# Kernel optimization log

Measured on AMD Instinct MI355X. Metric: run time of the kernel, lower is better.

## Reference

```python
import jax, jax.numpy as jnp
import numpy as np

BETA, GAMMA, ZETA = 0.66, -0.1, 1.1  # hard-concrete params
N, E, S = 20000, 640000, 256          # nodes, edges, samples (node feature dim)
D, P, PH, OUT = 2000, 500, 100, 2     # DEmRNA, pathway, pathway-hidden, out nodes


def setup_inputs() -> dict:
    key = jax.random.key(0)
    ks = jax.random.split(key, 14)
    return {
        "lnc_data": jax.random.normal(ks[0], (S, 8000), jnp.float32),
        "mi_data": jax.random.normal(ks[1], (S, 2000), jnp.float32),
        "m_data": jax.random.normal(ks[2], (S, 10000), jnp.float32),
        "src": jax.random.randint(ks[3], (E,), 0, N, dtype=jnp.int32),
        "dst": jax.random.randint(ks[4], (E,), 0, N, dtype=jnp.int32),
        "demrna_index": jax.random.randint(ks[5], (D,), 0, N, dtype=jnp.int32),
        "attn_l": jax.random.normal(ks[6], (N, 1), jnp.float32) * 0.01,
        "attn_r": jax.random.normal(ks[7], (N, 1), jnp.float32) * 0.01,
        "bias_l0": jnp.zeros((1,), jnp.float32),
        "pathway_mask": (jax.random.uniform(ks[8], (P, D)) < 0.1).astype(jnp.float32),
        "W_mp": jax.random.normal(ks[9], (P, D), jnp.float32) * (1.414 / np.sqrt(D)),
        "b_mp": jnp.zeros((P,), jnp.float32),
        "W_ph": jax.random.normal(ks[10], (PH, P), jnp.float32) * 0.05,
        "b_ph": jnp.zeros((PH,), jnp.float32),
        "W_po": jax.random.normal(ks[11], (OUT, PH), jnp.float32) * 0.1,
        "b_po": jnp.zeros((OUT,), jnp.float32),
    }


def _standardize(x):
    # torch pre_process: per-column (dim 0) mean/std, std unbiased (ddof=1)
    return (x - x.mean(axis=0)) / x.std(axis=0, ddof=1)


def reference(lnc_data, mi_data, m_data, src, dst, demrna_index,
              attn_l, attn_r, bias_l0, pathway_mask,
              W_mp, b_mp, W_ph, b_ph, W_po, b_po):
    rna = jnp.concatenate([lnc_data, mi_data, m_data], axis=1)  # [S, N]
    a_rna = _standardize(rna.T)                                  # [N, S] node feats

    # per-node attention logits (attn_l/r broadcast over sample dim)
    a1 = (a_rna * attn_l).sum(-1, keepdims=True)                 # [N, 1]
    a2 = (a_rna * attn_r).sum(-1, keepdims=True)                 # [N, 1]

    # edge attention with hard-concrete L0 gate (eval / l0_test path)
    logits = a1[src] + a2[dst] + bias_l0                         # [E, 1]
    s = jax.nn.sigmoid(logits / BETA)
    a = jnp.clip(s * (ZETA - GAMMA) + GAMMA, 0.0, 1.0)

    # custom edge-softmax: normalize by per-dst sum of gates
    z = jax.ops.segment_sum(a, dst, num_segments=N)              # [N, 1]
    a = a / z[dst]
    a = jnp.where(jnp.isnan(a), 0.0, a)                          # 0/0 -> 0

    # two rounds of u_mul_e + sum scatter aggregation
    rna1 = jax.ops.segment_sum(a * a_rna[src], dst, num_segments=N)  # [N, S]
    rna2 = jax.ops.segment_sum(a * rna1[src], dst, num_segments=N)   # [N, S]

    x = (a_rna + rna1 + rna2).T[:, demrna_index]                 # [S, D]

    # pas_net pathway branch (weight masked by pathway_mask each forward)
    h = jax.nn.relu(x @ (W_mp * pathway_mask).T + b_mp)          # [S, P]
    h = jax.nn.relu(h @ W_ph.T + b_ph)                           # [S, PH]
    return jax.nn.softmax(h @ W_po.T + b_po, axis=1)             # [S, OUT]
```

## Files before the change

### kernel.cpp

```cpp
#include <hip/hip_runtime.h>

#define NN 20000
#define EE 640000
#define SS 256
#define DD 2000
#define PP 500
#define PHH 100
#define ZSPLIT 25
#define KCH 80
#define SUB 10

typedef unsigned short ushort_t;

__device__ __forceinline__ unsigned short f2bf(float f) {
  unsigned u = __float_as_uint(f);
  unsigned r = (u + 0x7FFFu + ((u >> 16) & 1u)) >> 16;
  return (unsigned short)r;
}
__device__ __forceinline__ float lo16(unsigned u) { return __uint_as_float(u << 16); }
__device__ __forceinline__ float hi16(unsigned u) { return __uint_as_float(u & 0xFFFF0000u); }

__global__ __launch_bounds__(256) void k_meanstd(
    const float* __restrict__ lnc, const float* __restrict__ mi,
    const float* __restrict__ mdat, float* __restrict__ mean,
    float* __restrict__ invstd) {
  int s = blockIdx.x, tid = threadIdx.x;
  double sum = 0.0, ssq = 0.0;
  const float4* L = (const float4*)(lnc + (size_t)s * 8000);
  const float4* M = (const float4*)(mi + (size_t)s * 2000);
  const float4* D = (const float4*)(mdat + (size_t)s * 10000);
  for (int i = tid; i < 2000; i += 256) {
    float4 v = L[i];
    sum += (double)v.x + (double)v.y + (double)v.z + (double)v.w;
    ssq += (double)v.x * v.x + (double)v.y * v.y + (double)v.z * v.z + (double)v.w * v.w;
  }
  for (int i = tid; i < 500; i += 256) {
    float4 v = M[i];
    sum += (double)v.x + (double)v.y + (double)v.z + (double)v.w;
    ssq += (double)v.x * v.x + (double)v.y * v.y + (double)v.z * v.z + (double)v.w * v.w;
  }
  for (int i = tid; i < 2500; i += 256) {
    float4 v = D[i];
    sum += (double)v.x + (double)v.y + (double)v.z + (double)v.w;
    ssq += (double)v.x * v.x + (double)v.y * v.y + (double)v.z * v.z + (double)v.w * v.w;
  }
  __shared__ double sm[256], sq[256];
  sm[tid] = sum; sq[tid] = ssq; __syncthreads();
  for (int o = 128; o > 0; o >>= 1) {
    if (tid < o) { sm[tid] += sm[tid + o]; sq[tid] += sq[tid + o]; }
    __syncthreads();
  }
  if (tid == 0) {
    double mu = sm[0] / 20000.0;
    double var = (sq[0] - 20000.0 * mu * mu) / 19999.0;
    mean[s] = (float)mu;
    invstd[s] = (float)(1.0 / sqrt(var));
  }
}

__global__ __launch_bounds__(256) void k_prep(
    const float* __restrict__ lnc, const float* __restrict__ mi,
    const float* __restrict__ mdat, const float* __restrict__ mean,
    const float* __restrict__ invstd, ushort_t* __restrict__ a_rna,
    float* __restrict__ rowsum4, const float* __restrict__ Wmp,
    const float* __restrict__ pmask, float* __restrict__ Wt,
    int* __restrict__ counts) {
  int b = blockIdx.x;
  int tx = threadIdx.x, ty = threadIdx.y;
  if (b < 2500) {
    __shared__ float tile[64][33];
    __shared__ float red[8][33];
    int nb = (b % 625) * 32, sb = (b / 625) * 64;
    int n = nb + tx;
    const float* base; int w, c;
    if (n < 8000)       { base = lnc;  w = 8000;  c = n; }
    else if (n < 10000) { base = mi;   w = 2000;  c = n - 8000; }
    else                { base = mdat; w = 10000; c = n - 10000; }
    for (int r = ty; r < 64; r += 8) {
      int s = sb + r;
      tile[r][tx] = (base[(size_t)s * w + c] - mean[s]) * invstd[s];
    }
    __syncthreads();
    float ps = 0.f;
    for (int r = ty; r < 64; r += 8) ps += tile[r][tx];
    red[ty][tx] = ps;
    __syncthreads();
    if (ty == 0) {
      float t = 0.f;
      #pragma unroll
      for (int j = 0; j < 8; ++j) t += red[j][tx];
      rowsum4[(size_t)(sb >> 6) * NN + nb + tx] = t;
    }
    ushort2* out2 = (ushort2*)a_rna;
    for (int r2 = ty; r2 < 32; r2 += 8) {
      int nn = nb + r2;
      ushort2 v;
      v.x = f2bf(tile[2 * tx][r2]);
      v.y = f2bf(tile[2 * tx + 1][r2]);
      out2[(size_t)nn * 128 + (sb >> 1) + tx] = v;
    }
  } else if (b < 3508) {
    __shared__ float tile[32][33];
    int b2 = b - 2500;
    int p0 = (b2 & 15) * 32, d0 = (b2 >> 4) * 32;
    for (int r = ty; r < 32; r += 8) {
      int p = p0 + r, d = d0 + tx;
      float v = 0.f;
      if (p < PP && d < DD) v = Wmp[(size_t)p * DD + d] * pmask[(size_t)p * DD + d];
      tile[r][tx] = v;
    }
    __syncthreads();
    for (int r = ty; r < 32; r += 8) {
      int d = d0 + r, p = p0 + tx;
      if (d < DD) Wt[(size_t)d * 512 + p] = tile[tx][r];
    }
  } else {
    int b3 = b - 3508;
    int idx = b3 * 256 + ty * 32 + tx;
    if (idx < NN / 4) {
      uint4 z; z.x = 0; z.y = 0; z.z = 0; z.w = 0;
      ((uint4*)counts)[idx] = z;
    }
  }
}

__global__ __launch_bounds__(256) void k_count2(
    const int* __restrict__ dst, int* __restrict__ counts,
    const float* __restrict__ rowsum4, const float* __restrict__ attnl,
    const float* __restrict__ attnr, float* __restrict__ a1, float* __restrict__ a2) {
  int b = blockIdx.x;
  if (b < 2500) {
    int e = b * 256 + threadIdx.x;
    if (e < EE) atomicAdd(&counts[dst[e]], 1);
  } else {
    int n = (b - 2500) * 256 + threadIdx.x;
    if (n < NN) {
      float t = rowsum4[n] + rowsum4[NN + n] + rowsum4[2 * NN + n] + rowsum4[3 * NN + n];
      a1[n] = attnl[n] * t;
      a2[n] = attnr[n] * t;
    }
  }
}

__global__ __launch_bounds__(1024) void k_scan(
    const int* __restrict__ counts, int* __restrict__ offsets, int* __restrict__ cursor) {
  __shared__ int sums[1024];
  int t = threadIdx.x;
  int base = t * 20;
  int local[20];
  int s = 0;
  for (int i = 0; i < 20; ++i) {
    int idx = base + i;
    int c = (idx < NN) ? counts[idx] : 0;
    local[i] = s; s += c;
  }
  sums[t] = s; __syncthreads();
  for (int d = 1; d < 1024; d <<= 1) {
    int v = (t >= d) ? sums[t - d] : 0;
    __syncthreads();
    sums[t] += v;
    __syncthreads();
  }
  int prefix = (t > 0) ? sums[t - 1] : 0;
  for (int i = 0; i < 20; ++i) {
    int idx = base + i;
    if (idx < NN) { int o = prefix + local[i]; offsets[idx] = o; cursor[idx] = o; }
  }
  if (t == 1023) offsets[NN] = sums[1023];
}

__device__ __forceinline__ float hc_gate(float l) {
  float sg = 1.0f / (1.0f + __expf(-l * 1.5151515151f));
  return fminf(fmaxf(fmaf(sg, 1.2f, -0.1f), 0.0f), 1.0f);
}

__global__ __launch_bounds__(256) void k_fill(
    const int* __restrict__ src, const int* __restrict__ dst,
    const float* __restrict__ a1, const float* __restrict__ a2,
    const float* __restrict__ bias0, int* __restrict__ cursor,
    uint2* __restrict__ csr) {
  int e = blockIdx.x * 256 + threadIdx.x;
  if (e >= EE) return;
  int d = dst[e], s = src[e];
  float a = hc_gate(a1[s] + a2[d] + bias0[0]);
  int slot = atomicAdd(&cursor[d], 1);
  uint2 rec; rec.x = (unsigned)s; rec.y = __float_as_uint(a);
  csr[slot] = rec;
}

__global__ __launch_bounds__(256) void k_agg(
    const uint2* __restrict__ csr, const int* __restrict__ offs,
    const ushort_t* __restrict__ in_bf, ushort_t* __restrict__ out_bf,
    float* __restrict__ zinv) {
  int wave = threadIdx.x >> 6, lane = threadIdx.x & 63;
  int half = lane >> 5, sl = lane & 31;
  int n = blockIdx.x * 4 + wave;
  int beg = __builtin_amdgcn_readfirstlane(offs[n]);
  int end = __builtin_amdgcn_readfirstlane(offs[n + 1]);
  float zp = 0.f;
  for (int i = beg + lane; i < end; i += 64) zp += __uint_as_float(csr[i].y);
  #pragma unroll
  for (int o = 1; o < 64; o <<= 1) zp += __shfl_xor(zp, o, 64);
  float inv = (zp > 0.f) ? 1.0f / zp : 0.0f;
  if (lane == 0) zinv[n] = inv;

  const uint4* in4 = (const uint4*)in_bf;
  float acc[8] = {0.f, 0.f, 0.f, 0.f, 0.f, 0.f, 0.f, 0.f};
  int i = beg;
  for (; i + 15 < end; i += 16) {
    uint2 r[8]; uint4 v[8];
    #pragma unroll
    for (int j = 0; j < 8; ++j) r[j] = csr[i + 2 * j + half];
    #pragma unroll
    for (int j = 0; j < 8; ++j) v[j] = in4[(size_t)r[j].x * 32 + sl];
    #pragma unroll
    for (int j = 0; j < 8; ++j) {
      float g = __uint_as_float(r[j].y) * inv;
      acc[0] += g * lo16(v[j].x); acc[1] += g * hi16(v[j].x);
      acc[2] += g * lo16(v[j].y); acc[3] += g * hi16(v[j].y);
      acc[4] += g * lo16(v[j].z); acc[5] += g * hi16(v[j].z);
      acc[6] += g * lo16(v[j].w); acc[7] += g * hi16(v[j].w);
    }
  }
  for (; i + 3 < end; i += 4) {
    uint2 rA = csr[i + half];
    uint2 rB = csr[i + 2 + half];
    uint4 vA = in4[(size_t)rA.x * 32 + sl];
    uint4 vB = in4[(size_t)rB.x * 32 + sl];
    float gA = __uint_as_float(rA.y) * inv, gB = __uint_as_float(rB.y) * inv;
    acc[0] += gA * lo16(vA.x) + gB * lo16(vB.x);
    acc[1] += gA * hi16(vA.x) + gB * hi16(vB.x);
    acc[2] += gA * lo16(vA.y) + gB * lo16(vB.y);
    acc[3] += gA * hi16(vA.y) + gB * hi16(vB.y);
    acc[4] += gA * lo16(vA.z) + gB * lo16(vB.z);
    acc[5] += gA * hi16(vA.z) + gB * hi16(vB.z);
    acc[6] += gA * lo16(vA.w) + gB * lo16(vB.w);
    acc[7] += gA * hi16(vA.w) + gB * hi16(vB.w);
  }
  for (; i + 1 < end; i += 2) {
    uint2 rA = csr[i + half];
    uint4 vA = in4[(size_t)rA.x * 32 + sl];
    float gA = __uint_as_float(rA.y) * inv;
    acc[0] += gA * lo16(vA.x); acc[1] += gA * hi16(vA.x);
    acc[2] += gA * lo16(vA.y); acc[3] += gA * hi16(vA.y);
    acc[4] += gA * lo16(vA.z); acc[5] += gA * hi16(vA.z);
    acc[6] += gA * lo16(vA.w); acc[7] += gA * hi16(vA.w);
  }
  if (i < end && half == 0) {
    uint2 rA = csr[i];
    uint4 vA = in4[(size_t)rA.x * 32 + sl];
    float gA = __uint_as_float(rA.y) * inv;
    acc[0] += gA * lo16(vA.x); acc[1] += gA * hi16(vA.x);
    acc[2] += gA * lo16(vA.y); acc[3] += gA * hi16(vA.y);
    acc[4] += gA * lo16(vA.z); acc[5] += gA * hi16(vA.z);
    acc[6] += gA * lo16(vA.w); acc[7] += gA * hi16(vA.w);
  }
  #pragma unroll
  for (int j = 0; j < 8; ++j) acc[j] += __shfl_xor(acc[j], 32, 64);
  if (half == 0) {
    uint4 w;
    w.x = (unsigned)f2bf(acc[0]) | ((unsigned)f2bf(acc[1]) << 16);
    w.y = (unsigned)f2bf(acc[2]) | ((unsigned)f2bf(acc[3]) << 16);
    w.z = (unsigned)f2bf(acc[4]) | ((unsigned)f2bf(acc[5]) << 16);
    w.w = (unsigned)f2bf(acc[6]) | ((unsigned)f2bf(acc[7]) << 16);
    ((uint4*)out_bf)[(size_t)n * 32 + sl] = w;
  }
}

__global__ __launch_bounds__(256) void k_pass2x(
    const int* __restrict__ dem, const int* __restrict__ offs,
    const uint2* __restrict__ csr, const ushort_t* __restrict__ a_rna,
    const ushort_t* __restrict__ rna1, const float* __restrict__ zinv,
    float* __restrict__ xt) {
  int wave = threadIdx.x >> 6, lane = threadIdx.x & 63;
  int half = lane >> 5, sl = lane & 31;
  int d = blockIdx.x * 4 + wave;
  int nd = dem[d];
  const uint4* ar = (const uint4*)a_rna;
  const uint4* r1 = (const uint4*)rna1;
  int beg = __builtin_amdgcn_readfirstlane(offs[nd]);
  int end = __builtin_amdgcn_readfirstlane(offs[nd + 1]);
  float inv = zinv[nd];
  float acc[8] = {0.f, 0.f, 0.f, 0.f, 0.f, 0.f, 0.f, 0.f};
  int i = beg;
  for (; i + 3 < end; i += 4) {
    uint2 rA = csr[i + half];
    uint2 rB = csr[i + 2 + half];
    uint4 vA = r1[(size_t)rA.x * 32 + sl];
    uint4 vB = r1[(size_t)rB.x * 32 + sl];
    float gA = __uint_as_float(rA.y) * inv, gB = __uint_as_float(rB.y) * inv;
    acc[0] += gA * lo16(vA.x) + gB * lo16(vB.x);
    acc[1] += gA * hi16(vA.x) + gB * hi16(vB.x);
    acc[2] += gA * lo16(vA.y) + gB * lo16(vB.y);
    acc[3] += gA * hi16(vA.y) + gB * hi16(vB.y);
    acc[4] += gA * lo16(vA.z) + gB * lo16(vB.z);
    acc[5] += gA * hi16(vA.z) + gB * hi16(vB.z);
    acc[6] += gA * lo16(vA.w) + gB * lo16(vB.w);
    acc[7] += gA * hi16(vA.w) + gB * hi16(vB.w);
  }
  for (; i + 1 < end; i += 2) {
    uint2 rA = csr[i + half];
    uint4 vA = r1[(size_t)rA.x * 32 + sl];
    float gA = __uint_as_float(rA.y) * inv;
    acc[0] += gA * lo16(vA.x); acc[1] += gA * hi16(vA.x);
    acc[2] += gA * lo16(vA.y); acc[3] += gA * hi16(vA.y);
    acc[4] += gA * lo16(vA.z); acc[5] += gA * hi16(vA.z);
    acc[6] += gA * lo16(vA.w); acc[7] += gA * hi16(vA.w);
  }
  if (i < end && half == 0) {
    uint2 rA = csr[i];
    uint4 vA = r1[(size_t)rA.x * 32 + sl];
    float gA = __uint_as_float(rA.y) * inv;
    acc[0] += gA * lo16(vA.x); acc[1] += gA * hi16(vA.x);
    acc[2] += gA * lo16(vA.y); acc[3] += gA * hi16(vA.y);
    acc[4] += gA * lo16(vA.z); acc[5] += gA * hi16(vA.z);
    acc[6] += gA * lo16(vA.w); acc[7] += gA * hi16(vA.w);
  }
  #pragma unroll
  for (int j = 0; j < 8; ++j) acc[j] += __shfl_xor(acc[j], 32, 64);
  if (half == 0) {
    uint4 va = ar[(size_t)nd * 32 + sl];
    uint4 vb = r1[(size_t)nd * 32 + sl];
    acc[0] += lo16(va.x) + lo16(vb.x); acc[1] += hi16(va.x) + hi16(vb.x);
    acc[2] += lo16(va.y) + lo16(vb.y); acc[3] += hi16(va.y) + hi16(vb.y);
    acc[4] += lo16(va.z) + lo16(vb.z); acc[5] += hi16(va.z) + hi16(vb.z);
    acc[6] += lo16(va.w) + lo16(vb.w); acc[7] += hi16(va.w) + hi16(vb.w);
    float4* xo = (float4*)&xt[(size_t)d * SS + sl * 8];
    float4 w0; w0.x = acc[0]; w0.y = acc[1]; w0.z = acc[2]; w0.w = acc[3];
    float4 w1; w1.x = acc[4]; w1.y = acc[5]; w1.z = acc[6]; w1.w = acc[7];
    xo[0] = w0; xo[1] = w1;
  }
}

__global__ __launch_bounds__(256) void k_gemm1(
    const float* __restrict__ xt, const float* __restrict__ Wt,
    float* __restrict__ partial) {
  __shared__ float As[SUB][64];
  __shared__ float Ws[SUB][68];
  int tid = threadIdx.x;
  int s0 = blockIdx.x * 64, p0 = blockIdx.y * 64, d0 = blockIdx.z * KCH;
  int ts = tid & 15, tp = tid >> 4;
  float acc[4][4];
  #pragma unroll
  for (int i = 0; i < 4; ++i)
    #pragma unroll
    for (int j = 0; j < 4; ++j) acc[i][j] = 0.f;

  for (int kt = 0; kt < KCH / SUB; ++kt) {
    int dd = d0 + kt * SUB;
    #pragma unroll
    for (int i = tid; i < SUB * 64; i += 256) {
      int r = i >> 6, c = i & 63;
      As[r][c] = xt[(size_t)(dd + r) * SS + s0 + c];
    }
    #pragma unroll
    for (int i = tid; i < SUB * 64; i += 256) {
      int r = i >> 6, c = i & 63;
      Ws[r][c] = Wt[(size_t)(dd + r) * 512 + p0 + c];
    }
    __syncthreads();
    #pragma unroll
    for (int kk = 0; kk < SUB; ++kk) {
      float4 a = *(const float4*)&As[kk][ts * 4];
      float4 b = *(const float4*)&Ws[kk][tp * 4];
      acc[0][0] += a.x * b.x; acc[0][1] += a.x * b.y; acc[0][2] += a.x * b.z; acc[0][3] += a.x * b.w;
      acc[1][0] += a.y * b.x; acc[1][1] += a.y * b.y; acc[1][2] += a.y * b.z; acc[1][3] += a.y * b.w;
      acc[2][0] += a.z * b.x; acc[2][1] += a.z * b.y; acc[2][2] += a.z * b.z; acc[2][3] += a.z * b.w;
      acc[3][0] += a.w * b.x; acc[3][1] += a.w * b.y; acc[3][2] += a.w * b.z; acc[3][3] += a.w * b.w;
    }
    __syncthreads();
  }
  float* dstp = partial + (size_t)blockIdx.z * 512 * 256;
  #pragma unroll
  for (int j = 0; j < 4; ++j) {
    int p = p0 + tp * 4 + j;
    float4 w; w.x = acc[0][j]; w.y = acc[1][j]; w.z = acc[2][j]; w.w = acc[3][j];
    *(float4*)&dstp[(size_t)p * 256 + s0 + ts * 4] = w;
  }
}

__global__ __launch_bounds__(256) void k_reduce(
    const float* __restrict__ partial, const float* __restrict__ bmp,
    float* __restrict__ h1t) {
  int idx4 = blockIdx.x * 256 + threadIdx.x;
  if (idx4 >= PP * SS / 4) return;
  int p = idx4 >> 6;
  float b = bmp[p];
  float4 acc; acc.x = b; acc.y = b; acc.z = b; acc.w = b;
  #pragma unroll
  for (int z = 0; z < ZSPLIT; ++z) {
    float4 v = ((const float4*)partial)[(size_t)z * 512 * 64 + idx4];
    acc.x += v.x; acc.y += v.y; acc.z += v.z; acc.w += v.w;
  }
  acc.x = fmaxf(acc.x, 0.f); acc.y = fmaxf(acc.y, 0.f);
  acc.z = fmaxf(acc.z, 0.f); acc.w = fmaxf(acc.w, 0.f);
  ((float4*)h1t)[idx4] = acc;
}

__global__ __launch_bounds__(64) void k_h2(
    const float* __restrict__ h1t, const float* __restrict__ Wph,
    const float* __restrict__ bph, float* __restrict__ h2t) {
  int ph = blockIdx.x;
  int s = blockIdx.y * 64 + threadIdx.x;
  const float* w = &Wph[(size_t)ph * PP];
  float acc[10];
  #pragma unroll
  for (int j = 0; j < 10; ++j) acc[j] = 0.f;
  for (int k = 0; k < 50; ++k) {
    int p = k * 10;
    #pragma unroll
    for (int j = 0; j < 10; ++j)
      acc[j] = fmaf(h1t[(size_t)(p + j) * SS + s], w[p + j], acc[j]);
  }
  float t = ((acc[0] + acc[1]) + (acc[2] + acc[3])) + ((acc[4] + acc[5]) + (acc[6] + acc[7])) + (acc[8] + acc[9]);
  h2t[(size_t)ph * SS + s] = fmaxf(t + bph[ph], 0.0f);
}

__global__ __launch_bounds__(256) void k_out(
    const float* __restrict__ h2t, const float* __restrict__ Wpo,
    const float* __restrict__ bpo, float* __restrict__ out) {
  int s = threadIdx.x;
  float o0 = bpo[0], o1 = bpo[1];
  for (int ph = 0; ph < PHH; ++ph) {
    float v = h2t[(size_t)ph * SS + s];
    o0 += v * Wpo[ph];
    o1 += v * Wpo[PHH + ph];
  }
  float mx = fmaxf(o0, o1);
  float e0 = __expf(o0 - mx), e1 = __expf(o1 - mx);
  float inv = 1.0f / (e0 + e1);
  out[2 * s] = e0 * inv;
  out[2 * s + 1] = e1 * inv;
}

extern "C" void kernel_launch(void* const* d_in, const int* in_sizes, int n_in,
                              void* d_out, int out_size, void* d_ws, size_t ws_size,
                              hipStream_t stream) {
  const float* lnc   = (const float*)d_in[0];
  const float* mi    = (const float*)d_in[1];
  const float* mdat  = (const float*)d_in[2];
  const int*   src   = (const int*)d_in[3];
  const int*   dst   = (const int*)d_in[4];
  const int*   dem   = (const int*)d_in[5];
  const float* attnl = (const float*)d_in[6];
  const float* attnr = (const float*)d_in[7];
  const float* bias0 = (const float*)d_in[8];
  const float* pmask = (const float*)d_in[9];
  const float* Wmp   = (const float*)d_in[10];
  const float* bmp   = (const float*)d_in[11];
  const float* Wph   = (const float*)d_in[12];
  const float* bph   = (const float*)d_in[13];
  const float* Wpo   = (const float*)d_in[14];
  const float* bpo   = (const float*)d_in[15];
  float* out = (float*)d_out;

  char* ws = (char*)d_ws;
  size_t off = 0;
  auto alloc = [&](size_t bytes) -> char* {
    char* p = ws + off;
    off += (bytes + 255) & ~(size_t)255;
    return p;
  };
  float*    mean    = (float*)alloc(SS * 4);
  float*    invstd  = (float*)alloc(SS * 4);
  float*    a1      = (float*)alloc(NN * 4);
  float*    a2      = (float*)alloc(NN * 4);
  float*    rowsum4 = (float*)alloc((size_t)4 * NN * 4);
  float*    zinv    = (float*)alloc(NN * 4);
  int*      counts  = (int*)alloc(NN * 4);
  int*      offs    = (int*)alloc((NN + 1) * 4);
  int*      cursor  = (int*)alloc(NN * 4);
  uint2*    csr     = (uint2*)alloc((size_t)EE * 8);
  ushort_t* a_rna   = (ushort_t*)alloc((size_t)NN * SS * 2);
  ushort_t* rna1    = (ushort_t*)alloc((size_t)NN * SS * 2);
  float*    xt      = (float*)alloc((size_t)DD * SS * 4);
  float*    Wt      = (float*)alloc((size_t)DD * 512 * 4);
  float*    partial = (float*)alloc((size_t)ZSPLIT * 512 * 256 * 4);
  float*    h1t     = (float*)alloc((size_t)PP * SS * 4);
  float*    h2t     = (float*)alloc((size_t)PHH * SS * 4);

  k_meanstd<<<SS, 256, 0, stream>>>(lnc, mi, mdat, mean, invstd);
  k_prep<<<3528, dim3(32, 8), 0, stream>>>(lnc, mi, mdat, mean, invstd, a_rna,
                                           rowsum4, Wmp, pmask, Wt, counts);
  k_count2<<<2579, 256, 0, stream>>>(dst, counts, rowsum4, attnl, attnr, a1, a2);
  k_scan<<<1, 1024, 0, stream>>>(counts, offs, cursor);
  k_fill<<<(EE + 255) / 256, 256, 0, stream>>>(src, dst, a1, a2, bias0, cursor, csr);
  k_agg<<<NN / 4, 256, 0, stream>>>(csr, offs, a_rna, rna1, zinv);
  k_pass2x<<<DD / 4, 256, 0, stream>>>(dem, offs, csr, a_rna, rna1, zinv, xt);
  k_gemm1<<<dim3(SS / 64, 8, ZSPLIT), 256, 0, stream>>>(xt, Wt, partial);
  k_reduce<<<(PP * SS / 4 + 255) / 256, 256, 0, stream>>>(partial, bmp, h1t);
  k_h2<<<dim3(PHH, SS / 64), 64, 0, stream>>>(h1t, Wph, bph, h2t);
  k_out<<<1, SS, 0, stream>>>(h2t, Wpo, bpo, out);
}
```

Measured before the change: 201.7 us.

## Regroup preprocessing kernels and fold gate normalization into aggregation

Reorganizes the front-end launch sequence. Weight masking/transpose and counts zeroing now run alongside the mean/std kernel, and the dst-count atomics move into the standardize kernel. The a1/a2 attention products are computed inside the scan launch, which cuts one kernel launch and its boundary. In the first aggregation pass, the per-destination gate sum is accumulated during the main loop instead of a separate pre-pass over the CSR gates, and normalization is applied once at output. This removes an extra CSR read per node, at the cost of slightly different rounding order.

New measurement: 198.6 us (median of 2 runs). No clear change (-1.5%).

```diff
diff --git a/kernel.cpp b/kernel.cpp
--- a/kernel.cpp
+++ b/kernel.cpp
@@ -20,41 +20,69 @@
 __device__ __forceinline__ float lo16(unsigned u) { return __uint_as_float(u << 16); }
 __device__ __forceinline__ float hi16(unsigned u) { return __uint_as_float(u & 0xFFFF0000u); }
 
-__global__ __launch_bounds__(256) void k_meanstd(
+__global__ __launch_bounds__(256) void k_pre(
     const float* __restrict__ lnc, const float* __restrict__ mi,
     const float* __restrict__ mdat, float* __restrict__ mean,
-    float* __restrict__ invstd) {
-  int s = blockIdx.x, tid = threadIdx.x;
-  double sum = 0.0, ssq = 0.0;
-  const float4* L = (const float4*)(lnc + (size_t)s * 8000);
-  const float4* M = (const float4*)(mi + (size_t)s * 2000);
-  const float4* D = (const float4*)(mdat + (size_t)s * 10000);
-  for (int i = tid; i < 2000; i += 256) {
-    float4 v = L[i];
-    sum += (double)v.x + (double)v.y + (double)v.z + (double)v.w;
-    ssq += (double)v.x * v.x + (double)v.y * v.y + (double)v.z * v.z + (double)v.w * v.w;
-  }
-  for (int i = tid; i < 500; i += 256) {
-    float4 v = M[i];
-    sum += (double)v.x + (double)v.y + (double)v.z + (double)v.w;
-    ssq += (double)v.x * v.x + (double)v.y * v.y + (double)v.z * v.z + (double)v.w * v.w;
-  }
-  for (int i = tid; i < 2500; i += 256) {
-    float4 v = D[i];
-    sum += (double)v.x + (double)v.y + (double)v.z + (double)v.w;
-    ssq += (double)v.x * v.x + (double)v.y * v.y + (double)v.z * v.z + (double)v.w * v.w;
-  }
-  __shared__ double sm[256], sq[256];
-  sm[tid] = sum; sq[tid] = ssq; __syncthreads();
-  for (int o = 128; o > 0; o >>= 1) {
-    if (tid < o) { sm[tid] += sm[tid + o]; sq[tid] += sq[tid + o]; }
+    float* __restrict__ invstd, const float* __restrict__ Wmp,
+    const float* __restrict__ pmask, float* __restrict__ Wt,
+    int* __restrict__ counts) {
+  int b = blockIdx.x;
+  int tx = threadIdx.x, ty = threadIdx.y;
+  int tid = ty * 32 + tx;
+  if (b < 256) {
+    int s = b;
+    double sum = 0.0, ssq = 0.0;
+    const float4* L = (const float4*)(lnc + (size_t)s * 8000);
+    const float4* M = (const float4*)(mi + (size_t)s * 2000);
+    const float4* D = (const float4*)(mdat + (size_t)s * 10000);
+    for (int i = tid; i < 2000; i += 256) {
+      float4 v = L[i];
+      sum += (double)v.x + (double)v.y + (double)v.z + (double)v.w;
+      ssq += (double)v.x * v.x + (double)v.y * v.y + (double)v.z * v.z + (double)v.w * v.w;
+    }
+    for (int i = tid; i < 500; i += 256) {
+      float4 v = M[i];
+      sum += (double)v.x + (double)v.y + (double)v.z + (double)v.w;
+      ssq += (double)v.x * v.x + (double)v.y * v.y + (double)v.z * v.z + (double)v.w * v.w;
+    }
+    for (int i = tid; i < 2500; i += 256) {
+      float4 v = D[i];
+      sum += (double)v.x + (double)v.y + (double)v.z + (double)v.w;
+      ssq += (double)v.x * v.x + (double)v.y * v.y + (double)v.z * v.z + (double)v.w * v.w;
+    }
+    __shared__ double sm[256], sq[256];
+    sm[tid] = sum; sq[tid] = ssq; __syncthreads();
+    for (int o = 128; o > 0; o >>= 1) {
+      if (tid < o) { sm[tid] += sm[tid + o]; sq[tid] += sq[tid + o]; }
+      __syncthreads();
+    }
+    if (tid == 0) {
+      double mu = sm[0] / 20000.0;
+      double var = (sq[0] - 20000.0 * mu * mu) / 19999.0;
+      mean[s] = (float)mu;
+      invstd[s] = (float)(1.0 / sqrt(var));
+    }
+  } else if (b < 1264) {
+    __shared__ float tile[32][33];
+    int b2 = b - 256;
+    int p0 = (b2 & 15) * 32, d0 = (b2 >> 4) * 32;
+    for (int r = ty; r < 32; r += 8) {
+      int p = p0 + r, d = d0 + tx;
+      float v = 0.f;
+      if (p < PP && d < DD) v = Wmp[(size_t)p * DD + d] * pmask[(size_t)p * DD + d];
+      tile[r][tx] = v;
+    }
     __syncthreads();
-  }
-  if (tid == 0) {
-    double mu = sm[0] / 20000.0;
-    double var = (sq[0] - 20000.0 * mu * mu) / 19999.0;
-    mean[s] = (float)mu;
-    invstd[s] = (float)(1.0 / sqrt(var));
+    for (int r = ty; r < 32; r += 8) {
+      int d = d0 + r, p = p0 + tx;
+      if (d < DD) Wt[(size_t)d * 512 + p] = tile[tx][r];
+    }
+  } else {
+    int idx = (b - 1264) * 256 + tid;
+    if (idx < NN / 4) {
+      uint4 z; z.x = 0; z.y = 0; z.z = 0; z.w = 0;
+      ((uint4*)counts)[idx] = z;
+    }
   }
 }
 
@@ -62,8 +90,7 @@
     const float* __restrict__ lnc, const float* __restrict__ mi,
     const float* __restrict__ mdat, const float* __restrict__ mean,
     const float* __restrict__ invstd, ushort_t* __restrict__ a_rna,
-    float* __restrict__ rowsum4, const float* __restrict__ Wmp,
-    const float* __restrict__ pmask, float* __restrict__ Wt,
+    float* __restrict__ rowsum4, const int* __restrict__ dst,
     int* __restrict__ counts) {
   int b = blockIdx.x;
   int tx = threadIdx.x, ty = threadIdx.y;
@@ -99,74 +126,48 @@
       v.y = f2bf(tile[2 * tx + 1][r2]);
       out2[(size_t)nn * 128 + (sb >> 1) + tx] = v;
     }
-  } else if (b < 3508) {
-    __shared__ float tile[32][33];
-    int b2 = b - 2500;
-    int p0 = (b2 & 15) * 32, d0 = (b2 >> 4) * 32;
-    for (int r = ty; r < 32; r += 8) {
-      int p = p0 + r, d = d0 + tx;
-      float v = 0.f;
-      if (p < PP && d < DD) v = Wmp[(size_t)p * DD + d] * pmask[(size_t)p * DD + d];
-      tile[r][tx] = v;
-    }
-    __syncthreads();
-    for (int r = ty; r < 32; r += 8) {
-      int d = d0 + r, p = p0 + tx;
-      if (d < DD) Wt[(size_t)d * 512 + p] = tile[tx][r];
-    }
   } else {
-    int b3 = b - 3508;
-    int idx = b3 * 256 + ty * 32 + tx;
-    if (idx < NN / 4) {
-      uint4 z; z.x = 0; z.y = 0; z.z = 0; z.w = 0;
-      ((uint4*)counts)[idx] = z;
-    }
-  }
-}
-
-__global__ __launch_bounds__(256) void k_count2(
-    const int* __restrict__ dst, int* __restrict__ counts,
+    int e = (b - 2500) * 256 + ty * 32 + tx;
+    if (e < EE) atomicAdd(&counts[dst[e]], 1);
+  }
+}
+
+__global__ __launch_bounds__(1024) void k_scan(
+    const int* __restrict__ counts, int* __restrict__ offsets, int* __restrict__ cursor,
     const float* __restrict__ rowsum4, const float* __restrict__ attnl,
     const float* __restrict__ attnr, float* __restrict__ a1, float* __restrict__ a2) {
-  int b = blockIdx.x;
-  if (b < 2500) {
-    int e = b * 256 + threadIdx.x;
-    if (e < EE) atomicAdd(&counts[dst[e]], 1);
+  if (blockIdx.x == 0) {
+    __shared__ int sums[1024];
+    int t = threadIdx.x;
+    int base = t * 20;
+    int local[20];
+    int s = 0;
+    for (int i = 0; i < 20; ++i) {
+      int idx = base + i;
+      int c = (idx < NN) ? counts[idx] : 0;
+      local[i] = s; s += c;
+    }
+    sums[t] = s; __syncthreads();
+    for (int d = 1; d < 1024; d <<= 1) {
+      int v = (t >= d) ? sums[t - d] : 0;
+      __syncthreads();
+      sums[t] += v;
+      __syncthreads();
+    }
+    int prefix = (t > 0) ? sums[t - 1] : 0;
+    for (int i = 0; i < 20; ++i) {
+      int idx = base + i;
+      if (idx < NN) { int o = prefix + local[i]; offsets[idx] = o; cursor[idx] = o; }
+    }
+    if (t == 1023) offsets[NN] = sums[1023];
   } else {
-    int n = (b - 2500) * 256 + threadIdx.x;
+    int n = (blockIdx.x - 1) * 1024 + threadIdx.x;
     if (n < NN) {
       float t = rowsum4[n] + rowsum4[NN + n] + rowsum4[2 * NN + n] + rowsum4[3 * NN + n];
       a1[n] = attnl[n] * t;
       a2[n] = attnr[n] * t;
     }
   }
-}
-
-__global__ __launch_bounds__(1024) void k_scan(
-    const int* __restrict__ counts, int* __restrict__ offsets, int* __restrict__ cursor) {
-  __shared__ int sums[1024];
-  int t = threadIdx.x;
-  int base = t * 20;
-  int local[20];
-  int s = 0;
-  for (int i = 0; i < 20; ++i) {
-    int idx = base + i;
-    int c = (idx < NN) ? counts[idx] : 0;
-    local[i] = s; s += c;
-  }
-  sums[t] = s; __syncthreads();
-  for (int d = 1; d < 1024; d <<= 1) {
-    int v = (t >= d) ? sums[t - d] : 0;
-    __syncthreads();
-    sums[t] += v;
-    __syncthreads();
-  }
-  int prefix = (t > 0) ? sums[t - 1] : 0;
-  for (int i = 0; i < 20; ++i) {
-    int idx = base + i;
-    if (idx < NN) { int o = prefix + local[i]; offsets[idx] = o; cursor[idx] = o; }
-  }
-  if (t == 1023) offsets[NN] = sums[1023];
 }
 
 __device__ __forceinline__ float hc_gate(float l) {
@@ -197,15 +198,10 @@
   int n = blockIdx.x * 4 + wave;
   int beg = __builtin_amdgcn_readfirstlane(offs[n]);
   int end = __builtin_amdgcn_readfirstlane(offs[n + 1]);
-  float zp = 0.f;
-  for (int i = beg + lane; i < end; i += 64) zp += __uint_as_float(csr[i].y);
-  #pragma unroll
-  for (int o = 1; o < 64; o <<= 1) zp += __shfl_xor(zp, o, 64);
-  float inv = (zp > 0.f) ? 1.0f / zp : 0.0f;
-  if (lane == 0) zinv[n] = inv;
 
   const uint4* in4 = (const uint4*)in_bf;
   float acc[8] = {0.f, 0.f, 0.f, 0.f, 0.f, 0.f, 0.f, 0.f};
+  float zsum = 0.f;
   int i = beg;
   for (; i + 15 < end; i += 16) {
     uint2 r[8]; uint4 v[8];
@@ -215,7 +211,8 @@
     for (int j = 0; j < 8; ++j) v[j] = in4[(size_t)r[j].x * 32 + sl];
     #pragma unroll
     for (int j = 0; j < 8; ++j) {
-      float g = __uint_as_float(r[j].y) * inv;
+      float g = __uint_as_float(r[j].y);
+      zsum += g;
       acc[0] += g * lo16(v[j].x); acc[1] += g * hi16(v[j].x);
       acc[2] += g * lo16(v[j].y); acc[3] += g * hi16(v[j].y);
       acc[4] += g * lo16(v[j].z); acc[5] += g * hi16(v[j].z);
@@ -227,7 +224,8 @@
     uint2 rB = csr[i + 2 + half];
     uint4 vA = in4[(size_t)rA.x * 32 + sl];
     uint4 vB = in4[(size_t)rB.x * 32 + sl];
-    float gA = __uint_as_float(rA.y) * inv, gB = __uint_as_float(rB.y) * inv;
+    float gA = __uint_as_float(rA.y), gB = __uint_as_float(rB.y);
+    zsum += gA + gB;
     acc[0] += gA * lo16(vA.x) + gB * lo16(vB.x);
     acc[1] += gA * hi16(vA.x) + gB * hi16(vB.x);
     acc[2] += gA * lo16(vA.y) + gB * lo16(vB.y);
@@ -240,7 +238,8 @@
   for (; i + 1 < end; i += 2) {
     uint2 rA = csr[i + half];
     uint4 vA = in4[(size_t)rA.x * 32 + sl];
-    float gA = __uint_as_float(rA.y) * inv;
+    float gA = __uint_as_float(rA.y);
+    zsum += gA;
     acc[0] += gA * lo16(vA.x); acc[1] += gA * hi16(vA.x);
     acc[2] += gA * lo16(vA.y); acc[3] += gA * hi16(vA.y);
     acc[4] += gA * lo16(vA.z); acc[5] += gA * hi16(vA.z);
@@ -249,7 +248,8 @@
   if (i < end && half == 0) {
     uint2 rA = csr[i];
     uint4 vA = in4[(size_t)rA.x * 32 + sl];
-    float gA = __uint_as_float(rA.y) * inv;
+    float gA = __uint_as_float(rA.y);
+    zsum += gA;
     acc[0] += gA * lo16(vA.x); acc[1] += gA * hi16(vA.x);
     acc[2] += gA * lo16(vA.y); acc[3] += gA * hi16(vA.y);
     acc[4] += gA * lo16(vA.z); acc[5] += gA * hi16(vA.z);
@@ -257,12 +257,15 @@
   }
   #pragma unroll
   for (int j = 0; j < 8; ++j) acc[j] += __shfl_xor(acc[j], 32, 64);
+  float z = zsum + __shfl_xor(zsum, 32, 64);
+  float inv = (z > 0.f) ? 1.0f / z : 0.0f;
+  if (lane == 0) zinv[n] = inv;
   if (half == 0) {
     uint4 w;
-    w.x = (unsigned)f2bf(acc[0]) | ((unsigned)f2bf(acc[1]) << 16);
-    w.y = (unsigned)f2bf(acc[2]) | ((unsigned)f2bf(acc[3]) << 16);
-    w.z = (unsigned)f2bf(acc[4]) | ((unsigned)f2bf(acc[5]) << 16);
-    w.w = (unsigned)f2bf(acc[6]) | ((unsigned)f2bf(acc[7]) << 16);
+    w.x = (unsigned)f2bf(acc[0] * inv) | ((unsigned)f2bf(acc[1] * inv) << 16);
+    w.y = (unsigned)f2bf(acc[2] * inv) | ((unsigned)f2bf(acc[3] * inv) << 16);
+    w.z = (unsigned)f2bf(acc[4] * inv) | ((unsigned)f2bf(acc[5] * inv) << 16);
+    w.w = (unsigned)f2bf(acc[6] * inv) | ((unsigned)f2bf(acc[7] * inv) << 16);
     ((uint4*)out_bf)[(size_t)n * 32 + sl] = w;
   }
 }
@@ -479,11 +482,9 @@
   float*    h1t     = (float*)alloc((size_t)PP * SS * 4);
   float*    h2t     = (float*)alloc((size_t)PHH * SS * 4);
 
-  k_meanstd<<<SS, 256, 0, stream>>>(lnc, mi, mdat, mean, invstd);
-  k_prep<<<3528, dim3(32, 8), 0, stream>>>(lnc, mi, mdat, mean, invstd, a_rna,
-                                           rowsum4, Wmp, pmask, Wt, counts);
-  k_count2<<<2579, 256, 0, stream>>>(dst, counts, rowsum4, attnl, attnr, a1, a2);
-  k_scan<<<1, 1024, 0, stream>>>(counts, offs, cursor);
+  k_pre<<<1284, dim3(32, 8), 0, stream>>>(lnc, mi, mdat, mean, invstd, Wmp, pmask, Wt, counts);
+  k_prep<<<5000, dim3(32, 8), 0, stream>>>(lnc, mi, mdat, mean, invstd, a_rna, rowsum4, dst, counts);
+  k_scan<<<21, 1024, 0, stream>>>(counts, offs, cursor, rowsum4, attnl, attnr, a1, a2);
   k_fill<<<(EE + 255) / 256, 256, 0, stream>>>(src, dst, a1, a2, bias0, cursor, csr);
   k_agg<<<NN / 4, 256, 0, stream>>>(csr, offs, a_rna, rna1, zinv);
   k_pass2x<<<DD / 4, 256, 0, stream>>>(dem, offs, csr, a_rna, rna1, zinv, xt);
```
